# Kernel optimization log

Measured on AMD Instinct MI355X. Metric: run time of the kernel, lower is better.

Reference implementation:

```python
import jax, jax.numpy as jnp
import numpy as np
import math

B, S, D, H = 2, 2048, 1024, 16
DH = D // H
FF = 4096
EPS = 1e-5


def _xavier(k, shape):
    lim = math.sqrt(6.0 / (shape[0] + shape[1]))
    return jax.random.uniform(k, shape, jnp.float32, -lim, lim)


def setup_inputs() -> dict:
    key = jax.random.key(0)
    ks = jax.random.split(key, 8)
    return {
        "x": jax.random.normal(ks[0], (B, S, D), jnp.float32),
        "mask": jnp.ones((B, S), jnp.int32),
        "WQ": _xavier(ks[1], (D, D)), "bQ": jnp.zeros((D,), jnp.float32),
        "WK": _xavier(ks[2], (D, D)), "bK": jnp.zeros((D,), jnp.float32),
        "WV": _xavier(ks[3], (D, D)), "bV": jnp.zeros((D,), jnp.float32),
        "WY": _xavier(ks[4], (D, D)), "bY": jnp.zeros((D,), jnp.float32),
        "ln1_w": jnp.ones((D,), jnp.float32), "ln1_b": jnp.zeros((D,), jnp.float32),
        "ln2_w": jnp.ones((D,), jnp.float32), "ln2_b": jnp.zeros((D,), jnp.float32),
        "W1": _xavier(ks[5], (D, FF)), "b1": jnp.zeros((FF,), jnp.float32),
        "W2": _xavier(ks[6], (FF, D)), "b2": jnp.zeros((D,), jnp.float32),
    }


def _layer_norm(x, w, b):
    # manual LayerNorm: biased variance over last dim
    m = jnp.mean(x, axis=-1, keepdims=True)
    v = jnp.mean(jnp.square(x - m), axis=-1, keepdims=True)
    return (x - m) / jnp.sqrt(v + EPS) * w + b


def _attention(x, mask, WQ, bQ, WK, bK, WV, bV, WY, bY):
    b, s, _ = x.shape
    def split(t):  # (B,S,D) -> (B,H,S,DH)
        return t.reshape(b, s, H, DH).transpose(0, 2, 1, 3)
    q = split(x @ WQ + bQ)
    k = split(x @ WK + bK)
    v = split(x @ WV + bV)
    scores = jnp.einsum('bhqd,bhkd->bhqk', q, k) / math.sqrt(DH)
    scores = jnp.where(mask[:, None, None, :] == 0, -jnp.inf, scores)
    w = jax.nn.softmax(scores, axis=-1)
    y = jnp.einsum('bhqk,bhkd->bhqd', w, v)
    y = y.transpose(0, 2, 1, 3).reshape(b, s, D)  # merge heads
    return y @ WY + bY


def reference(x, mask, WQ, bQ, WK, bK, WV, bV, WY, bY,
              ln1_w, ln1_b, ln2_w, ln2_b, W1, b1, W2, b2):
    a = _attention(x, mask, WQ, bQ, WK, bK, WV, bV, WY, bY)
    h = _layer_norm(a + x, ln1_w, ln1_b)
    ff = jax.nn.gelu(h @ W1 + b1, approximate=False) @ W2 + b2
    return _layer_norm(ff + h, ln2_w, ln2_b)
```

## Files before the change

### kernel.cpp

```cpp
#include <hip/hip_runtime.h>
#include <cstdint>
#include <cstddef>

#define B_ 2
#define S_ 2048
#define D_ 1024
#define H_ 16
#define DH_ 64
#define FF_ 4096
#define M_ (B_*S_)
#define MB_ ((size_t)1 << 20)
#define NT_ (S_/64)

using u16 = unsigned short;
using short8 = __attribute__((ext_vector_type(8))) short;
using short4v = __attribute__((ext_vector_type(4))) short;
using floatx4 = __attribute__((ext_vector_type(4))) float;

__device__ __forceinline__ float bf2f(u16 u) {
    return __uint_as_float(((uint32_t)u) << 16);
}
__device__ __forceinline__ u16 f2bf(float f) {
    uint32_t u = __float_as_uint(f);
    u += 0x7fffu + ((u >> 16) & 1u);
    return (u16)(u >> 16);
}
__device__ __forceinline__ uint32_t cvtpk_bf16(float lo, float hi) {
    uint32_t r;
    asm("v_cvt_pk_bf16_f32 %0, %1, %2" : "=v"(r) : "v"(lo), "v"(hi));
    return r;
}
__device__ __forceinline__ void async_copy16(const u16* g, u16* l) {
    __builtin_amdgcn_global_load_lds(
        (const __attribute__((address_space(1))) uint32_t*)g,
        (__attribute__((address_space(3))) uint32_t*)l, 16, 0, 0);
}

__global__ __launch_bounds__(256) void cvt_f32_bf16(
    const float* __restrict__ in, u16* __restrict__ out, int n)
{
    const int i = (blockIdx.x * 256 + threadIdx.x) * 4;
    if (i < n) {
        const float4 v = *(const float4*)(in + i);
        out[i + 0] = f2bf(v.x);
        out[i + 1] = f2bf(v.y);
        out[i + 2] = f2bf(v.z);
        out[i + 3] = f2bf(v.w);
    }
}

__global__ __launch_bounds__(256) void mask_bias(
    const int* __restrict__ mask, float* __restrict__ bias, int n)
{
    const int i = blockIdx.x * 256 + threadIdx.x;
    if (i < n) bias[i] = mask[i] ? 0.f : -1e30f;
}

__global__ void transpose_cvt(const float* __restrict__ in, u16* __restrict__ out,
                              int R, int C) {
    __shared__ float t[32][33];
    const int bx = blockIdx.x * 32, by = blockIdx.y * 32;
    const int tx = threadIdx.x, ty = threadIdx.y;
#pragma unroll
    for (int i = 0; i < 32; i += 8)
        t[ty + i][tx] = in[(size_t)(by + ty + i) * C + bx + tx];
    __syncthreads();
#pragma unroll
    for (int i = 0; i < 32; i += 8)
        out[(size_t)(bx + ty + i) * R + by + tx] = f2bf(t[tx][ty + i]);
}

__global__ void transpose_cvt4(
    const float* __restrict__ WQ, const float* __restrict__ WK,
    const float* __restrict__ WV, const float* __restrict__ WY,
    u16* __restrict__ Wqkvt, u16* __restrict__ WYt)
{
    __shared__ float t[32][33];
    const int zz = blockIdx.z;
    const float* in = zz == 0 ? WQ : zz == 1 ? WK : zz == 2 ? WV : WY;
    u16* out = zz < 3 ? Wqkvt + (size_t)zz * D_ * D_ : WYt;
    const int bx = blockIdx.x * 32, by = blockIdx.y * 32;
    const int tx = threadIdx.x, ty = threadIdx.y;
#pragma unroll
    for (int i = 0; i < 32; i += 8)
        t[ty + i][tx] = in[(size_t)(by + ty + i) * D_ + bx + tx];
    __syncthreads();
#pragma unroll
    for (int i = 0; i < 32; i += 8)
        out[(size_t)(bx + ty + i) * D_ + by + tx] = f2bf(t[tx][ty + i]);
}

template<bool GELU, bool OUT_F32>
__global__ __launch_bounds__(256) void gemm_bt(
    const u16* __restrict__ A, const u16* __restrict__ Bt,
    const float* __restrict__ bias, void* __restrict__ Cout,
    int M, int N, int K)
{
    __shared__ alignas(16) u16 As[128 * 32];
    __shared__ alignas(16) u16 Bs[128 * 32];
    const int tid = threadIdx.x;
    const int w = tid >> 6, lane = tid & 63;
    const int lm = lane & 15, quad = lane >> 4;
    const int wm = w >> 1, wn = w & 1;
    const size_t m0 = (size_t)blockIdx.y * 128, n0 = (size_t)blockIdx.x * 128;

    const int rowS = w * 16 + (lane >> 2);
    const int colS = (lane & 3) * 8;
    const u16* gA = A + (m0 + rowS) * K + colS;
    const u16* gB = Bt + (n0 + rowS) * K + colS;
    u16* lA = As + w * 512;
    u16* lB = Bs + w * 512;

    floatx4 acc[4][4];
    const floatx4 z = {0.f, 0.f, 0.f, 0.f};
#pragma unroll
    for (int i = 0; i < 4; ++i)
#pragma unroll
        for (int j = 0; j < 4; ++j) acc[i][j] = z;

    for (int k0 = 0; k0 < K; k0 += 32) {
        __syncthreads();
        async_copy16(gA, lA);
        async_copy16(gA + (size_t)64 * K, lA + 2048);
        async_copy16(gB, lB);
        async_copy16(gB + (size_t)64 * K, lB + 2048);
        gA += 32; gB += 32;
        __syncthreads();

        short8 af[4], bfr[4];
#pragma unroll
        for (int t = 0; t < 4; ++t)
            af[t] = *(const short8*)&As[(wm * 64 + t * 16 + lm) * 32 + quad * 8];
#pragma unroll
        for (int t = 0; t < 4; ++t)
            bfr[t] = *(const short8*)&Bs[(wn * 64 + t * 16 + lm) * 32 + quad * 8];
#pragma unroll
        for (int i = 0; i < 4; ++i)
#pragma unroll
            for (int j = 0; j < 4; ++j)
                acc[i][j] = __builtin_amdgcn_mfma_f32_16x16x32_bf16(
                    af[i], bfr[j], acc[i][j], 0, 0, 0);
    }

#pragma unroll
    for (int i = 0; i < 4; ++i) {
        const size_t r0 = m0 + wm * 64 + i * 16 + quad * 4;
#pragma unroll
        for (int j = 0; j < 4; ++j) {
            const size_t c = n0 + wn * 64 + j * 16 + lm;
            const float bv = bias[c];
#pragma unroll
            for (int t = 0; t < 4; ++t) {
                float v = acc[i][j][t] + bv;
                if (GELU) v = 0.5f * v * (1.f + erff(v * 0.70710678118f));
                if (OUT_F32) ((float*)Cout)[(r0 + t) * (size_t)N + c] = v;
                else         ((u16*)Cout)[(r0 + t) * (size_t)N + c] = f2bf(v);
            }
        }
    }
}

__global__ __launch_bounds__(256) void gemm_bt_sk2(
    const u16* __restrict__ A, const u16* __restrict__ Bt,
    const float* __restrict__ bias, float* __restrict__ Cout,
    int M, int N, int K)
{
    __shared__ alignas(16) u16 As[128 * 32];
    __shared__ alignas(16) u16 Bs[128 * 32];
    const int tid = threadIdx.x;
    const int w = tid >> 6, lane = tid & 63;
    const int lm = lane & 15, quad = lane >> 4;
    const int wm = w >> 1, wn = w & 1;
    const int kh = blockIdx.z;
    const int Ks = K >> 1;
    const size_t m0 = (size_t)blockIdx.y * 128, n0 = (size_t)blockIdx.x * 128;

    const int rowS = w * 16 + (lane >> 2);
    const int colS = (lane & 3) * 8;
    const u16* gA = A + (m0 + rowS) * K + (size_t)kh * Ks + colS;
    const u16* gB = Bt + (n0 + rowS) * K + (size_t)kh * Ks + colS;
    u16* lA = As + w * 512;
    u16* lB = Bs + w * 512;

    floatx4 acc[4][4];
    const floatx4 z = {0.f, 0.f, 0.f, 0.f};
#pragma unroll
    for (int i = 0; i < 4; ++i)
#pragma unroll
        for (int j = 0; j < 4; ++j) acc[i][j] = z;

    for (int k0 = 0; k0 < Ks; k0 += 32) {
        __syncthreads();
        async_copy16(gA, lA);
        async_copy16(gA + (size_t)64 * K, lA + 2048);
        async_copy16(gB, lB);
        async_copy16(gB + (size_t)64 * K, lB + 2048);
        gA += 32; gB += 32;
        __syncthreads();

        short8 af[4], bfr[4];
#pragma unroll
        for (int t = 0; t < 4; ++t)
            af[t] = *(const short8*)&As[(wm * 64 + t * 16 + lm) * 32 + quad * 8];
#pragma unroll
        for (int t = 0; t < 4; ++t)
            bfr[t] = *(const short8*)&Bs[(wn * 64 + t * 16 + lm) * 32 + quad * 8];
#pragma unroll
        for (int i = 0; i < 4; ++i)
#pragma unroll
            for (int j = 0; j < 4; ++j)
                acc[i][j] = __builtin_amdgcn_mfma_f32_16x16x32_bf16(
                    af[i], bfr[j], acc[i][j], 0, 0, 0);
    }

#pragma unroll
    for (int i = 0; i < 4; ++i) {
        const size_t r0 = m0 + wm * 64 + i * 16 + quad * 4;
#pragma unroll
        for (int j = 0; j < 4; ++j) {
            const size_t c = n0 + wn * 64 + j * 16 + lm;
            const float bv = (kh == 0) ? bias[c] : 0.f;
#pragma unroll
            for (int t = 0; t < 4; ++t)
                atomicAdd(&Cout[(r0 + t) * (size_t)N + c], acc[i][j][t] + bv);
        }
    }
}

__global__ __launch_bounds__(256) void gemm_qkv(
    const u16* __restrict__ A, const u16* __restrict__ Bt,
    const float* __restrict__ bQ, const float* __restrict__ bK,
    const float* __restrict__ bV,
    u16* __restrict__ Qb, u16* __restrict__ Kb, u16* __restrict__ Vt)
{
    const int K = D_, N = 3 * D_;
    __shared__ alignas(16) u16 As[128 * 32];
    __shared__ alignas(16) u16 Bs[128 * 32];
    const int tid = threadIdx.x;
    const int w = tid >> 6, lane = tid & 63;
    const int lm = lane & 15, quad = lane >> 4;
    const int wm = w >> 1, wn = w & 1;
    const size_t m0 = (size_t)blockIdx.y * 128, n0 = (size_t)blockIdx.x * 128;

    const int rowS = w * 16 + (lane >> 2);
    const int colS = (lane & 3) * 8;
    const u16* gA = A + (m0 + rowS) * K + colS;
    const u16* gB = Bt + (n0 + rowS) * K + colS;
    u16* lA = As + w * 512;
    u16* lB = Bs + w * 512;

    floatx4 acc[4][4];
    const floatx4 z = {0.f, 0.f, 0.f, 0.f};
#pragma unroll
    for (int i = 0; i < 4; ++i)
#pragma unroll
        for (int j = 0; j < 4; ++j) acc[i][j] = z;

    for (int k0 = 0; k0 < K; k0 += 32) {
        __syncthreads();
        async_copy16(gA, lA);
        async_copy16(gA + (size_t)64 * K, lA + 2048);
        async_copy16(gB, lB);
        async_copy16(gB + (size_t)64 * K, lB + 2048);
        gA += 32; gB += 32;
        __syncthreads();

        short8 af[4], bfr[4];
#pragma unroll
        for (int t = 0; t < 4; ++t)
            af[t] = *(const short8*)&As[(wm * 64 + t * 16 + lm) * 32 + quad * 8];
#pragma unroll
        for (int t = 0; t < 4; ++t)
            bfr[t] = *(const short8*)&Bs[(wn * 64 + t * 16 + lm) * 32 + quad * 8];
#pragma unroll
        for (int i = 0; i < 4; ++i)
#pragma unroll
            for (int j = 0; j < 4; ++j)
                acc[i][j] = __builtin_amdgcn_mfma_f32_16x16x32_bf16(
                    af[i], bfr[j], acc[i][j], 0, 0, 0);
    }

#pragma unroll
    for (int i = 0; i < 4; ++i) {
        const size_t r0 = m0 + wm * 64 + i * 16 + quad * 4;
#pragma unroll
        for (int j = 0; j < 4; ++j) {
            const size_t c = n0 + wn * 64 + j * 16 + lm;
            const int sel = (int)(c >> 10);
            const int col = (int)(c & 1023);
            const float bv = sel == 0 ? bQ[col] : (sel == 1 ? bK[col] : bV[col]);
#pragma unroll
            for (int t = 0; t < 4; ++t) {
                const size_t r = r0 + t;
                const u16 v = f2bf(acc[i][j][t] + bv);
                if (sel == 0)      Qb[r * (size_t)D_ + col] = v;
                else if (sel == 1) Kb[r * (size_t)D_ + col] = v;
                else {
                    const int h = col >> 6, dh = col & 63;
                    const int bb = (int)(r >> 11), s = (int)(r & 2047);
                    Vt[((size_t)((bb * 16 + h) * 64 + dh)) * S_ + s] = v;
                }
            }
        }
    }
}

__global__ __launch_bounds__(256) void attn_kernel(
    const u16* __restrict__ Q, const u16* __restrict__ Kg,
    const u16* __restrict__ Vt, const float* __restrict__ mbias,
    u16* __restrict__ O)
{
    __shared__ alignas(16) u16 Kt[2][64 * 72];
    __shared__ alignas(16) u16 Vs[2][64 * 72];
    const int tid = threadIdx.x, w = tid >> 6, lane = tid & 63;
    const int lm = lane & 15, quad = lane >> 4;
    const int b = blockIdx.y >> 4, h = blockIdx.y & 15;
    const int q0 = blockIdx.x * 64;

    const u16* qp = Q + ((size_t)(b * S_ + q0 + w * 16 + lm)) * D_ + h * 64;
    const short8 bq0 = *(const short8*)(qp + quad * 8);
    const short8 bq1 = *(const short8*)(qp + 32 + quad * 8);

    const int sRow = tid >> 2, sCol = (tid & 3) * 16;
    const u16* gK = Kg + ((size_t)(b * S_ + sRow)) * D_ + h * 64 + sCol;
    const u16* gV = Vt + ((size_t)((b * 16 + h) * 64 + sRow)) * S_ + sCol;

    float mrow = -1e30f, lrow = 0.f;
    floatx4 o[4];
    const floatx4 z = {0.f, 0.f, 0.f, 0.f};
#pragma unroll
    for (int i = 0; i < 4; ++i) o[i] = z;

    const float* bp = mbias + b * S_;
    const float SCL = 0.18033688011112042f;

    short8 rk0 = *(const short8*)(gK);
    short8 rk1 = *(const short8*)(gK + 8);
    short8 rv0 = *(const short8*)(gV);
    short8 rv1 = *(const short8*)(gV + 8);

    for (int it = 0; it < NT_; ++it) {
        u16* kb = Kt[it & 1];
        u16* vb = Vs[it & 1];
        *(short8*)&kb[sRow * 72 + sCol]     = rk0;
        *(short8*)&kb[sRow * 72 + sCol + 8] = rk1;
        *(short8*)&vb[sRow * 72 + sCol]     = rv0;
        *(short8*)&vb[sRow * 72 + sCol + 8] = rv1;
        __syncthreads();
        if (it + 1 < NT_) {
            gK += (size_t)64 * D_; gV += 64;
            rk0 = *(const short8*)(gK);
            rk1 = *(const short8*)(gK + 8);
            rv0 = *(const short8*)(gV);
            rv1 = *(const short8*)(gV + 8);
        }

        floatx4 st[4];
        __builtin_amdgcn_s_setprio(1);
#pragma unroll
        for (int ks = 0; ks < 4; ++ks) {
            floatx4 s = z;
            const short8 ak0 = *(const short8*)&kb[(ks * 16 + lm) * 72 + quad * 8];
            const short8 ak1 = *(const short8*)&kb[(ks * 16 + lm) * 72 + 32 + quad * 8];
            s = __builtin_amdgcn_mfma_f32_16x16x32_bf16(ak0, bq0, s, 0, 0, 0);
            s = __builtin_amdgcn_mfma_f32_16x16x32_bf16(ak1, bq1, s, 0, 0, 0);
            const float4 mb4 = *(const float4*)&bp[it * 64 + ks * 16 + quad * 4];
            st[ks][0] = fmaf(s[0], SCL, mb4.x);
            st[ks][1] = fmaf(s[1], SCL, mb4.y);
            st[ks][2] = fmaf(s[2], SCL, mb4.z);
            st[ks][3] = fmaf(s[3], SCL, mb4.w);
        }
        __builtin_amdgcn_s_setprio(0);

        float t0 = fmaxf(fmaxf(st[0][0], st[0][1]), st[0][2]);
        float t1 = fmaxf(fmaxf(st[0][3], st[1][0]), st[1][1]);
        float t2 = fmaxf(fmaxf(st[1][2], st[1][3]), st[2][0]);
        float t3 = fmaxf(fmaxf(st[2][1], st[2][2]), st[2][3]);
        float t4 = fmaxf(fmaxf(st[3][0], st[3][1]), st[3][2]);
        float tm = fmaxf(fmaxf(t0, t1), t2);
        tm = fmaxf(fmaxf(tm, t3), t4);
        tm = fmaxf(tm, st[3][3]);
        tm = fmaxf(tm, __shfl_xor(tm, 16));
        tm = fmaxf(tm, __shfl_xor(tm, 32));

        if (!__all(tm <= mrow + 8.f)) {
            const float mn = fmaxf(mrow, tm);
            const float al = __builtin_amdgcn_exp2f(mrow - mn);
            mrow = mn;
            lrow *= al;
#pragma unroll
            for (int d = 0; d < 4; ++d) o[d] *= al;
        }

        float rs = 0.f;
#pragma unroll
        for (int ks = 0; ks < 4; ++ks)
#pragma unroll
            for (int r = 0; r < 4; ++r) {
                const float p = __builtin_amdgcn_exp2f(st[ks][r] - mrow);
                st[ks][r] = p; rs += p;
            }
        rs += __shfl_xor(rs, 16);
        rs += __shfl_xor(rs, 32);
        lrow += rs;

        short4v pb[4];
#pragma unroll
        for (int ks = 0; ks < 4; ++ks) {
            uint2 uu;
            uu.x = cvtpk_bf16(st[ks][0], st[ks][1]);
            uu.y = cvtpk_bf16(st[ks][2], st[ks][3]);
            pb[ks] = __builtin_bit_cast(short4v, uu);
        }
        __builtin_amdgcn_s_setprio(1);
#pragma unroll
        for (int d = 0; d < 4; ++d)
#pragma unroll
            for (int ks = 0; ks < 4; ++ks) {
                const short4v av = *(const short4v*)&vb[(d * 16 + lm) * 72 + ks * 16 + quad * 4];
                o[d] = __builtin_amdgcn_mfma_f32_16x16x16bf16_1k(av, pb[ks], o[d], 0, 0, 0);
            }
        __builtin_amdgcn_s_setprio(0);
    }
    const float inv = __builtin_amdgcn_rcpf(lrow);
    u16* op = O + ((size_t)(b * S_ + q0 + w * 16 + lm)) * D_ + h * 64 + quad * 4;
#pragma unroll
    for (int d = 0; d < 4; ++d) {
        uint2 uu;
        uu.x = cvtpk_bf16(o[d][0] * inv, o[d][1] * inv);
        uu.y = cvtpk_bf16(o[d][2] * inv, o[d][3] * inv);
        *(uint2*)(op + d * 16) = uu;
    }
}

template<bool MAIN_F32, bool RESID_F32, bool OUT_F32>
__global__ __launch_bounds__(256) void add_ln(
    const void* __restrict__ mainp, const void* __restrict__ resid,
    const float* __restrict__ gamma, const float* __restrict__ beta,
    void* __restrict__ out)
{
    const int row = blockIdx.x;
    const size_t base = (size_t)row * D_;
    const int t = threadIdx.x;
    const int w = t >> 6, lane = t & 63;
    float v[4];
#pragma unroll
    for (int i = 0; i < 4; ++i) {
        const int c = i * 256 + t;
        const float mv = MAIN_F32 ? ((const float*)mainp)[base + c]
                                  : bf2f(((const u16*)mainp)[base + c]);
        const float rv = RESID_F32 ? ((const float*)resid)[base + c]
                                   : bf2f(((const u16*)resid)[base + c]);
        v[i] = mv + rv;
    }
    float s = v[0] + v[1] + v[2] + v[3];
#pragma unroll
    for (int off = 32; off >= 1; off >>= 1) s += __shfl_xor(s, off);
    __shared__ float red[8];
    if (lane == 0) red[w] = s;
    __syncthreads();
    const float mean = (red[0] + red[1] + red[2] + red[3]) * (1.0f / D_);
    float q = 0.f;
#pragma unroll
    for (int i = 0; i < 4; ++i) { const float dd = v[i] - mean; q += dd * dd; }
#pragma unroll
    for (int off = 32; off >= 1; off >>= 1) q += __shfl_xor(q, off);
    if (lane == 0) red[4 + w] = q;
    __syncthreads();
    const float var = (red[4] + red[5] + red[6] + red[7]) * (1.0f / D_);
    const float rstd = rsqrtf(var + 1e-5f);
#pragma unroll
    for (int i = 0; i < 4; ++i) {
        const int c = i * 256 + t;
        const float o = (v[i] - mean) * rstd * gamma[c] + beta[c];
        if (OUT_F32) ((float*)out)[base + c] = o;
        else         ((u16*)out)[base + c] = f2bf(o);
    }
}

extern "C" void kernel_launch(void* const* d_in, const int* in_sizes, int n_in,
                              void* d_out, int out_size, void* d_ws, size_t ws_size,
                              hipStream_t stream)
{
    const float* x   = (const float*)d_in[0];
    const int* mask  = (const int*)d_in[1];
    const float* WQ = (const float*)d_in[2];  const float* bQ = (const float*)d_in[3];
    const float* WK = (const float*)d_in[4];  const float* bK = (const float*)d_in[5];
    const float* WV = (const float*)d_in[6];  const float* bV = (const float*)d_in[7];
    const float* WY = (const float*)d_in[8];  const float* bY = (const float*)d_in[9];
    const float* ln1w = (const float*)d_in[10]; const float* ln1b = (const float*)d_in[11];
    const float* ln2w = (const float*)d_in[12]; const float* ln2b = (const float*)d_in[13];
    const float* W1 = (const float*)d_in[14]; const float* b1 = (const float*)d_in[15];
    const float* W2 = (const float*)d_in[16]; const float* b2 = (const float*)d_in[17];

    char* ws = (char*)d_ws;
    u16* xb    = (u16*)(ws + 0  * MB_);
    u16* Wqkvt = (u16*)(ws + 8  * MB_);
    u16* WYt   = (u16*)(ws + 14 * MB_);
    u16* Qb    = (u16*)(ws + 16 * MB_);
    u16* Kb    = (u16*)(ws + 24 * MB_);
    u16* Vt    = (u16*)(ws + 32 * MB_);
    u16* Yat   = (u16*)(ws + 40 * MB_);
    float* Ypf = (float*)(ws + 16 * MB_);
    u16* hbf   = (u16*)(ws + 8  * MB_);
    u16* W1t   = (u16*)(ws + 0  * MB_);
    u16* G     = (u16*)(ws + 16 * MB_);
    u16* W2t   = (u16*)(ws + 0  * MB_);
    float* mb  = (float*)(ws + 48 * MB_);

    const dim3 tb(32, 8);

    cvt_f32_bf16<<<(M_*D_)/1024, 256, 0, stream>>>(x, xb, M_*D_);
    mask_bias<<<(B_*S_)/256, 256, 0, stream>>>(mask, mb, B_*S_);
    transpose_cvt4<<<dim3(D_/32, D_/32, 4), tb, 0, stream>>>(WQ, WK, WV, WY, Wqkvt, WYt);

    gemm_qkv<<<dim3(3*D_/128, M_/128), 256, 0, stream>>>(xb, Wqkvt, bQ, bK, bV, Qb, Kb, Vt);

    attn_kernel<<<dim3(S_/64, B_*H_), 256, 0, stream>>>(Qb, Kb, Vt, mb, Yat);

    hipMemsetAsync(Ypf, 0, (size_t)M_ * D_ * 4, stream);
    gemm_bt_sk2<<<dim3(D_/128, M_/128, 2), 256, 0, stream>>>(Yat, WYt, bY, Ypf, M_, D_, D_);

    add_ln<true,true,false><<<M_, 256, 0, stream>>>(Ypf, x, ln1w, ln1b, hbf);

    transpose_cvt<<<dim3(FF_/32, D_/32), tb, 0, stream>>>(W1, W1t, D_, FF_);
    gemm_bt<true,false><<<dim3(FF_/128, M_/128), 256, 0, stream>>>(hbf, W1t, b1, G, M_, FF_, D_);

    transpose_cvt<<<dim3(D_/32, FF_/32), tb, 0, stream>>>(W2, W2t, FF_, D_);
    hipMemsetAsync(d_out, 0, (size_t)M_ * D_ * 4, stream);
    gemm_bt_sk2<<<dim3(D_/128, M_/128, 2), 256, 0, stream>>>(G, W2t, b2, (float*)d_out, M_, D_, FF_);

    add_ln<true,false,true><<<M_, 256, 0, stream>>>((float*)d_out, hbf, ln2w, ln2b, d_out);
}
```

Baseline: 483.0 us.

## Replace atomic split-K with partial buffers reduced inside fused add-LayerNorm

Split-K GEMMs for the output projection and W2 now write each K-slice's partial result to its own fp32 buffer instead of zeroing the output and accumulating atomically. The partials are summed inside a new add_ln_red kernel that also adds the residual and applies LayerNorm. This removes the two memsets and the atomic traffic. The W2 GEMM uses a 4-way K split for more parallelism, and block indices are remapped for locality. In exchange it needs extra workspace and extra reads of the partial buffers in the LayerNorm pass, and it falls back to the old path when workspace is insufficient.

```diff
diff --git a/kernel.cpp b/kernel.cpp
--- a/kernel.cpp
+++ b/kernel.cpp
@@ -156,6 +156,82 @@
                 if (OUT_F32) ((float*)Cout)[(r0 + t) * (size_t)N + c] = v;
                 else         ((u16*)Cout)[(r0 + t) * (size_t)N + c] = f2bf(v);
             }
+        }
+    }
+}
+
+__global__ __launch_bounds__(256) void gemm_bt_skp(
+    const u16* __restrict__ A, const u16* __restrict__ Bt,
+    const float* __restrict__ bias, float* __restrict__ out0,
+    float* __restrict__ Pext, int M, int N, int K)
+{
+    __shared__ alignas(16) u16 As[128 * 32];
+    __shared__ alignas(16) u16 Bs[128 * 32];
+    const int tid = threadIdx.x;
+    const int w = tid >> 6, lane = tid & 63;
+    const int lm = lane & 15, quad = lane >> 4;
+    const int wm = w >> 1, wn = w & 1;
+    const int kh = blockIdx.z;
+    const int Ks = K / gridDim.z;
+
+    const int nwg = gridDim.x * gridDim.y;
+    int bid = blockIdx.y * gridDim.x + blockIdx.x;
+    if ((nwg & 7) == 0) {
+        const int cpx = nwg >> 3;
+        bid = (bid & 7) * cpx + (bid >> 3);
+    }
+    const int bx = bid % gridDim.x, by = bid / gridDim.x;
+    const size_t m0 = (size_t)by * 128, n0 = (size_t)bx * 128;
+
+    const int rowS = w * 16 + (lane >> 2);
+    const int colS = (lane & 3) * 8;
+    const u16* gA = A + (m0 + rowS) * K + (size_t)kh * Ks + colS;
+    const u16* gB = Bt + (n0 + rowS) * K + (size_t)kh * Ks + colS;
+    u16* lA = As + w * 512;
+    u16* lB = Bs + w * 512;
+
+    floatx4 acc[4][4];
+    const floatx4 z = {0.f, 0.f, 0.f, 0.f};
+#pragma unroll
+    for (int i = 0; i < 4; ++i)
+#pragma unroll
+        for (int j = 0; j < 4; ++j) acc[i][j] = z;
+
+    for (int k0 = 0; k0 < Ks; k0 += 32) {
+        __syncthreads();
+        async_copy16(gA, lA);
+        async_copy16(gA + (size_t)64 * K, lA + 2048);
+        async_copy16(gB, lB);
+        async_copy16(gB + (size_t)64 * K, lB + 2048);
+        gA += 32; gB += 32;
+        __syncthreads();
+
+        short8 af[4], bfr[4];
+#pragma unroll
+        for (int t = 0; t < 4; ++t)
+            af[t] = *(const short8*)&As[(wm * 64 + t * 16 + lm) * 32 + quad * 8];
+#pragma unroll
+        for (int t = 0; t < 4; ++t)
+            bfr[t] = *(const short8*)&Bs[(wn * 64 + t * 16 + lm) * 32 + quad * 8];
+#pragma unroll
+        for (int i = 0; i < 4; ++i)
+#pragma unroll
+            for (int j = 0; j < 4; ++j)
+                acc[i][j] = __builtin_amdgcn_mfma_f32_16x16x32_bf16(
+                    af[i], bfr[j], acc[i][j], 0, 0, 0);
+    }
+
+    float* Cout = (kh == 0) ? out0 : Pext + (size_t)(kh - 1) * ((size_t)M * N);
+#pragma unroll
+    for (int i = 0; i < 4; ++i) {
+        const size_t r0 = m0 + wm * 64 + i * 16 + quad * 4;
+#pragma unroll
+        for (int j = 0; j < 4; ++j) {
+            const size_t c = n0 + wn * 64 + j * 16 + lm;
+            const float bv = (kh == 0) ? bias[c] : 0.f;
+#pragma unroll
+            for (int t = 0; t < 4; ++t)
+                Cout[(r0 + t) * (size_t)N + c] = acc[i][j][t] + bv;
         }
     }
 }
@@ -452,6 +528,54 @@
         const float rv = RESID_F32 ? ((const float*)resid)[base + c]
                                    : bf2f(((const u16*)resid)[base + c]);
         v[i] = mv + rv;
+    }
+    float s = v[0] + v[1] + v[2] + v[3];
+#pragma unroll
+    for (int off = 32; off >= 1; off >>= 1) s += __shfl_xor(s, off);
+    __shared__ float red[8];
+    if (lane == 0) red[w] = s;
+    __syncthreads();
+    const float mean = (red[0] + red[1] + red[2] + red[3]) * (1.0f / D_);
+    float q = 0.f;
+#pragma unroll
+    for (int i = 0; i < 4; ++i) { const float dd = v[i] - mean; q += dd * dd; }
+#pragma unroll
+    for (int off = 32; off >= 1; off >>= 1) q += __shfl_xor(q, off);
+    if (lane == 0) red[4 + w] = q;
+    __syncthreads();
+    const float var = (red[4] + red[5] + red[6] + red[7]) * (1.0f / D_);
+    const float rstd = rsqrtf(var + 1e-5f);
+#pragma unroll
+    for (int i = 0; i < 4; ++i) {
+        const int c = i * 256 + t;
+        const float o = (v[i] - mean) * rstd * gamma[c] + beta[c];
+        if (OUT_F32) ((float*)out)[base + c] = o;
+        else         ((u16*)out)[base + c] = f2bf(o);
+    }
+}
+
+template<int NEXT, bool RESID_F32, bool OUT_F32>
+__global__ __launch_bounds__(256) void add_ln_red(
+    const float* __restrict__ mainp, const float* __restrict__ Pext,
+    const void* __restrict__ resid,
+    const float* __restrict__ gamma, const float* __restrict__ beta,
+    void* __restrict__ out)
+{
+    const int row = blockIdx.x;
+    const size_t base = (size_t)row * D_;
+    const int t = threadIdx.x;
+    const int w = t >> 6, lane = t & 63;
+    float v[4];
+#pragma unroll
+    for (int i = 0; i < 4; ++i) {
+        const int c = i * 256 + t;
+        float s = mainp[base + c];
+#pragma unroll
+        for (int p = 0; p < NEXT; ++p)
+            s += Pext[(size_t)p * ((size_t)M_ * D_) + base + c];
+        s += RESID_F32 ? ((const float*)resid)[base + c]
+                       : bf2f(((const u16*)resid)[base + c]);
+        v[i] = s;
     }
     float s = v[0] + v[1] + v[2] + v[3];
 #pragma unroll
@@ -507,6 +631,11 @@
     u16* G     = (u16*)(ws + 16 * MB_);
     u16* W2t   = (u16*)(ws + 0  * MB_);
     float* mb  = (float*)(ws + 48 * MB_);
+    float* Pext = (float*)(ws + 49 * MB_);
+
+    const size_t PART = (size_t)M_ * D_ * sizeof(float);
+    const bool ws1 = ws_size >= 49 * MB_ + 1 * PART;
+    const bool ws3 = ws_size >= 49 * MB_ + 3 * PART;
 
     const dim3 tb(32, 8);
 
@@ -518,17 +647,37 @@
 
     attn_kernel<<<dim3(S_/64, B_*H_), 256, 0, stream>>>(Qb, Kb, Vt, mb, Yat);
 
-    hipMemsetAsync(Ypf, 0, (size_t)M_ * D_ * 4, stream);
-    gemm_bt_sk2<<<dim3(D_/128, M_/128, 2), 256, 0, stream>>>(Yat, WYt, bY, Ypf, M_, D_, D_);
-
-    add_ln<true,true,false><<<M_, 256, 0, stream>>>(Ypf, x, ln1w, ln1b, hbf);
+    if (ws1) {
+        gemm_bt_skp<<<dim3(D_/128, M_/128, 2), 256, 0, stream>>>(
+            Yat, WYt, bY, Ypf, Pext, M_, D_, D_);
+        add_ln_red<1,true,false><<<M_, 256, 0, stream>>>(Ypf, Pext, x, ln1w, ln1b, hbf);
+    } else {
+        hipMemsetAsync(Ypf, 0, PART, stream);
+        gemm_bt_sk2<<<dim3(D_/128, M_/128, 2), 256, 0, stream>>>(
+            Yat, WYt, bY, Ypf, M_, D_, D_);
+        add_ln<true,true,false><<<M_, 256, 0, stream>>>(Ypf, x, ln1w, ln1b, hbf);
+    }
 
     transpose_cvt<<<dim3(FF_/32, D_/32), tb, 0, stream>>>(W1, W1t, D_, FF_);
     gemm_bt<true,false><<<dim3(FF_/128, M_/128), 256, 0, stream>>>(hbf, W1t, b1, G, M_, FF_, D_);
 
     transpose_cvt<<<dim3(D_/32, FF_/32), tb, 0, stream>>>(W2, W2t, FF_, D_);
-    hipMemsetAsync(d_out, 0, (size_t)M_ * D_ * 4, stream);
-    gemm_bt_sk2<<<dim3(D_/128, M_/128, 2), 256, 0, stream>>>(G, W2t, b2, (float*)d_out, M_, D_, FF_);
-
-    add_ln<true,false,true><<<M_, 256, 0, stream>>>((float*)d_out, hbf, ln2w, ln2b, d_out);
-}
+
+    if (ws3) {
+        gemm_bt_skp<<<dim3(D_/128, M_/128, 4), 256, 0, stream>>>(
+            G, W2t, b2, (float*)d_out, Pext, M_, D_, FF_);
+        add_ln_red<3,false,true><<<M_, 256, 0, stream>>>(
+            (float*)d_out, Pext, hbf, ln2w, ln2b, d_out);
+    } else if (ws1) {
+        gemm_bt_skp<<<dim3(D_/128, M_/128, 2), 256, 0, stream>>>(
+            G, W2t, b2, (float*)d_out, Pext, M_, D_, FF_);
+        add_ln_red<1,false,true><<<M_, 256, 0, stream>>>(
+            (float*)d_out, Pext, hbf, ln2w, ln2b, d_out);
+    } else {
+        hipMemsetAsync(d_out, 0, (size_t)M_ * D_ * 4, stream);
+        gemm_bt_sk2<<<dim3(D_/128, M_/128, 2), 256, 0, stream>>>(
+            G, W2t, b2, (float*)d_out, M_, D_, FF_);
+        add_ln<true,false,true><<<M_, 256, 0, stream>>>(
+            (float*)d_out, hbf, ln2w, ln2b, d_out);
+    }
+}
```

Result: faster. 458.5 us (-5.1%).
